# Optimization experiments

Hardware: AMD Instinct MI355X
Metric: run time of the kernel (lower is better)

Reference implementation:

```python
import jax, jax.numpy as jnp
import numpy as np

WS = 7          # window size
NH = 12         # num heads
DIM = 384       # embed dim
HD = DIM // NH  # head dim
BW = 2048       # B_ = batch * num_windows
N = WS * WS     # tokens per window


def _relative_position_index(ws):
    coords = np.stack(np.meshgrid(np.arange(ws), np.arange(ws), indexing='ij'))  # [2,ws,ws]
    cf = coords.reshape(2, -1)                      # [2, ws*ws]
    rel = cf[:, :, None] - cf[:, None, :]           # [2, N, N]
    rel = rel.transpose(1, 2, 0).copy()             # [N, N, 2]
    rel[:, :, 0] += ws - 1
    rel[:, :, 1] += ws - 1
    rel[:, :, 0] *= 2 * ws - 1
    return jnp.asarray(rel.sum(-1))                 # [N, N] int


REL_IDX = _relative_position_index(WS)


def setup_inputs() -> dict:
    key = jax.random.key(0)
    ks = jax.random.split(key, 6)
    return {
        'x': jax.random.normal(ks[0], (BW, N, DIM), dtype=jnp.float32),
        'qkv_w': jax.random.normal(ks[1], (3 * DIM, DIM), dtype=jnp.float32) * 0.02,
        'qkv_b': jax.random.normal(ks[2], (3 * DIM,), dtype=jnp.float32) * 0.02,
        'proj_w': jax.random.normal(ks[3], (DIM, DIM), dtype=jnp.float32) * 0.02,
        'proj_b': jax.random.normal(ks[4], (DIM,), dtype=jnp.float32) * 0.02,
        'rel_bias_table': jax.random.normal(ks[5], ((2 * WS - 1) ** 2, NH), dtype=jnp.float32) * 0.02,
    }


def reference(x, qkv_w, qkv_b, proj_w, proj_b, rel_bias_table):
    B_, n, c = x.shape
    scale = HD ** -0.5
    qkv = x @ qkv_w.T + qkv_b                                   # [B_, N, 3*DIM]
    qkv = qkv.reshape(B_, n, 3, NH, HD).transpose(2, 0, 3, 1, 4)  # [3, B_, H, N, HD]
    q, k, v = qkv[0], qkv[1], qkv[2]
    attn = jnp.einsum('bhnd,bhmd->bhnm', q * scale, k)           # [B_, H, N, N]
    bias = rel_bias_table[REL_IDX.reshape(-1)].reshape(n, n, NH)  # gather -> [N, N, H]
    attn = attn + bias.transpose(2, 0, 1)[None]                   # add [1, H, N, N]
    attn = jax.nn.softmax(attn, axis=-1)
    out = jnp.einsum('bhnm,bhmd->bhnd', attn, v)                 # [B_, H, N, HD]
    out = out.transpose(0, 2, 1, 3).reshape(B_, n, c)            # [B_, N, C]
    return out @ proj_w.T + proj_b
```

## Files before the change

kernel.cpp:

```cpp
#include <hip/hip_runtime.h>
#include <hip/hip_bf16.h>

#define NH 12
constexpr float SCALE = 0.17677669529663687f;
constexpr int TOKENS = 100352;

using f32x4  = __attribute__((ext_vector_type(4))) float;
using bf16x8 = __attribute__((ext_vector_type(8))) __bf16;

__device__ inline void gload_lds16(const void* g, void* l) {
  __builtin_amdgcn_global_load_lds(
      (const __attribute__((address_space(1))) void*)g,
      (__attribute__((address_space(3))) void*)l, 16, 0, 0);
}

__device__ inline bf16x8 cvt8(float4 a, float4 b) {
  bf16x8 o;
  o[0] = (__bf16)a.x; o[1] = (__bf16)a.y; o[2] = (__bf16)a.z; o[3] = (__bf16)a.w;
  o[4] = (__bf16)b.x; o[5] = (__bf16)b.y; o[6] = (__bf16)b.z; o[7] = (__bf16)b.w;
  return o;
}

#define MFMA(a, b, c) __builtin_amdgcn_mfma_f32_16x16x32_bf16(a, b, c, 0, 0, 0)

__global__ __launch_bounds__(256) void wa_prep(
    const float* __restrict__ qkv_w, const float* __restrict__ proj_w,
    const float* __restrict__ tbl,
    __bf16* __restrict__ qkv_w_bf, __bf16* __restrict__ proj_w_bf,
    float* __restrict__ biasTt) {
  int p = blockIdx.x * 256 + threadIdx.x;
  if (p < 442368) { qkv_w_bf[p] = (__bf16)qkv_w[p]; return; }
  p -= 442368;
  if (p < 147456) { proj_w_bf[p] = (__bf16)proj_w[p]; return; }
  p -= 147456;
  if (p >= 49152) return;
  int h = p >> 12, rem = p & 4095, j = rem >> 6, i = rem & 63;
  float v;
  if (j >= 49) v = -1e30f;
  else if (i >= 49) v = 0.0f;
  else {
    int py = i / 7, px = i % 7, qy = j / 7, qx = j % 7;
    v = tbl[((py - qy + 6) * 13 + (px - qx + 6)) * NH + h];
  }
  biasTt[p] = v;
}

__global__ __launch_bounds__(256, 4) void wa_qkv(
    const float* __restrict__ x, const __bf16* __restrict__ wq,
    const float* __restrict__ qkv_b, __bf16* __restrict__ qkv) {
  __shared__ __bf16 As[64 * 64];
  __shared__ __bf16 Bs[128 * 64];
  __shared__ __bf16 Cs[64 * 128];
  const int t = threadIdx.x, lane = t & 63, wv = t >> 6;
  const int lr = lane & 15, ls = lane >> 4;
  const int bid = blockIdx.x;
  const int q = bid / 72, rem = bid - q * 72;
  const int nb = rem >> 3, mb = q * 8 + (rem & 7);
  const int wr = wv >> 1, wc = wv & 1;
  f32x4 acc[2][4] = {};
  for (int kk = 0; kk < 6; ++kk) {
    if (kk) __syncthreads();
    float4 a0[2], a1[2];
    int rowA[2], cA[2];
    #pragma unroll
    for (int j = 0; j < 2; ++j) {
      int p = j * 256 + t;
      rowA[j] = p >> 3; cA[j] = p & 7;
      const float* src = x + (size_t)(mb * 64 + rowA[j]) * 384 + kk * 64 + cA[j] * 8;
      a0[j] = *(const float4*)src;
      a1[j] = *(const float4*)(src + 4);
    }
    #pragma unroll
    for (int j = 0; j < 4; ++j) {
      int p = j * 256 + t;
      int c = p >> 3, sl = p & 7;
      gload_lds16(wq + (size_t)(nb * 128 + c) * 384 + kk * 64 + (sl ^ (c & 7)) * 8,
                  Bs + p * 8);
    }
    #pragma unroll
    for (int j = 0; j < 2; ++j) {
      int cw = cA[j] ^ (rowA[j] & 7);
      *(bf16x8*)(As + rowA[j] * 64 + cw * 8) = cvt8(a0[j], a1[j]);
    }
    __syncthreads();
    #pragma unroll
    for (int ks = 0; ks < 2; ++ks) {
      bf16x8 af[2], bfr[4];
      #pragma unroll
      for (int rt = 0; rt < 2; ++rt) {
        int row = wr * 32 + rt * 16 + lr;
        af[rt] = *(const bf16x8*)(As + row * 64 + (((ks * 4 + ls) ^ (row & 7)) * 8));
      }
      #pragma unroll
      for (int ct = 0; ct < 4; ++ct) {
        int c = wc * 64 + ct * 16 + lr;
        bfr[ct] = *(const bf16x8*)(Bs + c * 64 + (((ks * 4 + ls) ^ (c & 7)) * 8));
      }
      #pragma unroll
      for (int rt = 0; rt < 2; ++rt)
        #pragma unroll
        for (int ct = 0; ct < 4; ++ct)
          acc[rt][ct] = MFMA(af[rt], bfr[ct], acc[rt][ct]);
    }
  }
  #pragma unroll
  for (int ct = 0; ct < 4; ++ct) {
    float b = qkv_b[nb * 128 + wc * 64 + ct * 16 + lr];
    #pragma unroll
    for (int rt = 0; rt < 2; ++rt)
      #pragma unroll
      for (int r = 0; r < 4; ++r) {
        int row = wr * 32 + rt * 16 + ls * 4 + r;
        Cs[row * 128 + wc * 64 + ct * 16 + lr] = (__bf16)(acc[rt][ct][r] + b);
      }
  }
  __syncthreads();
  #pragma unroll
  for (int j = 0; j < 4; ++j) {
    int p = j * 256 + t;
    int row = p >> 4, sub = p & 15;
    *(bf16x8*)(qkv + (size_t)(mb * 64 + row) * 1152 + nb * 128 + sub * 8) =
        *(const bf16x8*)(Cs + p * 8);
  }
}

__global__ __launch_bounds__(256, 3) void wa_attn(
    const float* __restrict__ biasTt, __bf16* __restrict__ qkv) {
  __shared__ __bf16 Pbuf[4][4096];
  __shared__ __bf16 Vbuf[4][2048];
  const int t = threadIdx.x, lane = t & 63, wv = t >> 6;
  const int lr = lane & 15, ls = lane >> 4;
  const int pair = blockIdx.x * 4 + wv;
  const int w = pair / NH, h = pair - w * NH;
  const int w49 = w * 49;
  __bf16* Pw = Pbuf[wv];
  __bf16* Vw = Vbuf[wv];
  f32x4 zero = {0.f, 0.f, 0.f, 0.f};
  bf16x8 ones;
  #pragma unroll
  for (int e = 0; e < 8; ++e) ones[e] = (__bf16)1.0f;

  {
    int row = lane;
    int tok = w49 + (row < 49 ? row : 48);
    const bf16x8* vsrc = (const bf16x8*)(qkv + (size_t)tok * 1152 + 768 + h * 32);
    int f = (row & 3) ^ ((row >> 3) & 3);
    #pragma unroll
    for (int c = 0; c < 4; ++c)
      *(bf16x8*)(Vw + row * 32 + ((c ^ f) * 8)) = vsrc[c];
  }
  bf16x8 qa[4], kb[4];
  #pragma unroll
  for (int rt = 0; rt < 4; ++rt) {
    int tok = min(w49 + rt * 16 + lr, TOKENS - 1);
    qa[rt] = *(const bf16x8*)(qkv + (size_t)tok * 1152 + h * 32 + ls * 8);
  }
  #pragma unroll
  for (int ct = 0; ct < 4; ++ct) {
    int tok = min(w49 + ct * 16 + lr, TOKENS - 1);
    kb[ct] = *(const bf16x8*)(qkv + (size_t)tok * 1152 + 384 + h * 32 + ls * 8);
  }
  f32x4 sacc[4][4];
  #pragma unroll
  for (int rt = 0; rt < 4; ++rt)
    #pragma unroll
    for (int ct = 0; ct < 4; ++ct)
      sacc[rt][ct] = MFMA(qa[rt], kb[ct], zero);
  #pragma unroll
  for (int rt = 0; rt < 4; ++rt) {
    int row0 = rt * 16 + ls * 4;
    #pragma unroll
    for (int ct = 0; ct < 4; ++ct) {
      int col = ct * 16 + lr;
      float4 bias = *(const float4*)(biasTt + (size_t)(h * 64 + col) * 64 + row0);
      #pragma unroll
      for (int r = 0; r < 4; ++r) {
        int row = row0 + r;
        float pr = __expf(fmaf(sacc[rt][ct][r], SCALE, ((const float*)&bias)[r]));
        Pw[row * 64 + (((col >> 3) ^ (row & 7)) * 8) + (col & 7)] = (__bf16)pr;
      }
    }
  }
  f32x4 oacc[4][2] = {};
  f32x4 osum[4] = {zero, zero, zero, zero};
  #pragma unroll
  for (int ks = 0; ks < 2; ++ks) {
    bf16x8 vb0, vb1;
    #pragma unroll
    for (int e = 0; e < 8; ++e) {
      int j = ks * 32 + ls * 8 + e;
      int a = j * 32 + (((lr >> 3) ^ (e & 3) ^ ls) * 8) + (lr & 7);
      vb0[e] = Vw[a];
      vb1[e] = Vw[a ^ 16];
    }
    #pragma unroll
    for (int rt = 0; rt < 4; ++rt) {
      int row = rt * 16 + lr;
      bf16x8 pa = *(const bf16x8*)(Pw + row * 64 + (((ks * 4 + ls) ^ (row & 7)) * 8));
      oacc[rt][0] = MFMA(pa, vb0, oacc[rt][0]);
      oacc[rt][1] = MFMA(pa, vb1, oacc[rt][1]);
      osum[rt]    = MFMA(pa, ones, osum[rt]);
    }
  }
  #pragma unroll
  for (int rt = 0; rt < 4; ++rt)
    #pragma unroll
    for (int r = 0; r < 4; ++r) {
      int row = rt * 16 + ls * 4 + r;
      if (row < 49) {
        float inv = 1.0f / osum[rt][r];
        __bf16* o = qkv + (size_t)(w49 + row) * 1152 + h * 32;
        o[lr]      = (__bf16)(oacc[rt][0][r] * inv);
        o[16 + lr] = (__bf16)(oacc[rt][1][r] * inv);
      }
    }
}

__global__ __launch_bounds__(256, 4) void wa_proj(
    const __bf16* __restrict__ qkv, const __bf16* __restrict__ pw,
    const float* __restrict__ proj_b, float* __restrict__ out) {
  __shared__ __bf16 As[64 * 64];
  __shared__ __bf16 Bs[128 * 64];
  const int t = threadIdx.x, lane = t & 63, wv = t >> 6;
  const int lr = lane & 15, ls = lane >> 4;
  const int bid = blockIdx.x;
  const int q = bid / 24, rem = bid - q * 24;
  const int nb = rem >> 3, mb = q * 8 + (rem & 7);
  const int wr = wv >> 1, wc = wv & 1;
  f32x4 acc[2][4] = {};
  for (int kk = 0; kk < 6; ++kk) {
    if (kk) __syncthreads();
    #pragma unroll
    for (int j = 0; j < 2; ++j) {
      int p = j * 256 + t;
      int row = p >> 3, sl = p & 7;
      gload_lds16(qkv + (size_t)(mb * 64 + row) * 1152 + kk * 64 + (sl ^ (row & 7)) * 8,
                  As + p * 8);
    }
    #pragma unroll
    for (int j = 0; j < 4; ++j) {
      int p = j * 256 + t;
      int c = p >> 3, sl = p & 7;
      gload_lds16(pw + (size_t)(nb * 128 + c) * 384 + kk * 64 + (sl ^ (c & 7)) * 8,
                  Bs + p * 8);
    }
    __syncthreads();
    #pragma unroll
    for (int ks = 0; ks < 2; ++ks) {
      bf16x8 af[2], bfr[4];
      #pragma unroll
      for (int rt = 0; rt < 2; ++rt) {
        int row = wr * 32 + rt * 16 + lr;
        af[rt] = *(const bf16x8*)(As + row * 64 + (((ks * 4 + ls) ^ (row & 7)) * 8));
      }
      #pragma unroll
      for (int ct = 0; ct < 4; ++ct) {
        int c = wc * 64 + ct * 16 + lr;
        bfr[ct] = *(const bf16x8*)(Bs + c * 64 + (((ks * 4 + ls) ^ (c & 7)) * 8));
      }
      #pragma unroll
      for (int rt = 0; rt < 2; ++rt)
        #pragma unroll
        for (int ct = 0; ct < 4; ++ct)
          acc[rt][ct] = MFMA(af[rt], bfr[ct], acc[rt][ct]);
    }
  }
  #pragma unroll
  for (int ct = 0; ct < 4; ++ct) {
    int col = nb * 128 + wc * 64 + ct * 16 + lr;
    float b = proj_b[col];
    #pragma unroll
    for (int rt = 0; rt < 2; ++rt)
      #pragma unroll
      for (int r = 0; r < 4; ++r) {
        int row = wr * 32 + rt * 16 + ls * 4 + r;
        out[(size_t)(mb * 64 + row) * 384 + col] = acc[rt][ct][r] + b;
      }
  }
}

extern "C" void kernel_launch(void* const* d_in, const int* in_sizes, int n_in,
                              void* d_out, int out_size, void* d_ws, size_t ws_size,
                              hipStream_t stream) {
  const float* x      = (const float*)d_in[0];
  const float* qkv_w  = (const float*)d_in[1];
  const float* qkv_b  = (const float*)d_in[2];
  const float* proj_w = (const float*)d_in[3];
  const float* proj_b = (const float*)d_in[4];
  const float* tbl    = (const float*)d_in[5];
  float* out = (float*)d_out;

  char* ws = (char*)d_ws;
  __bf16* qkv_w_bf  = (__bf16*)ws;
  __bf16* proj_w_bf = (__bf16*)(ws + 884736);
  float*  biasTt    = (float*)(ws + 1179648);
  __bf16* qkv_buf   = (__bf16*)(ws + 1376256);

  wa_prep<<<2496, 256, 0, stream>>>(qkv_w, proj_w, tbl, qkv_w_bf, proj_w_bf, biasTt);
  wa_qkv<<<14112, 256, 0, stream>>>(x, qkv_w_bf, qkv_b, qkv_buf);
  wa_attn<<<6144, 256, 0, stream>>>(biasTt, qkv_buf);
  wa_proj<<<4704, 256, 0, stream>>>(qkv_buf, proj_w_bf, proj_b, out);
}
```

Measured before the change: 336.5 us.

## Drop LDS staging in QKV and proj GEMMs, load MFMA fragments directly from global

Both projection GEMMs stop staging A and B tiles through shared memory with block-wide barriers. Each wave now loads its MFMA operand fragments straight from global memory (L2/L1) and keeps only a small per-wave LDS buffer for the coalesced output write in the QKV kernel. This removes the __syncthreads and LDS traffic per k-step, but each wave now fetches operand data that other waves in the block also fetch, and the loads are strided 16-byte per-lane rather than coalesced tiles.

```diff
diff --git a/kernel.cpp b/kernel.cpp
--- a/kernel.cpp
+++ b/kernel.cpp
@@ -7,12 +7,6 @@
 
 using f32x4  = __attribute__((ext_vector_type(4))) float;
 using bf16x8 = __attribute__((ext_vector_type(8))) __bf16;
-
-__device__ inline void gload_lds16(const void* g, void* l) {
-  __builtin_amdgcn_global_load_lds(
-      (const __attribute__((address_space(1))) void*)g,
-      (__attribute__((address_space(3))) void*)l, 16, 0, 0);
-}
 
 __device__ inline bf16x8 cvt8(float4 a, float4 b) {
   bf16x8 o;
@@ -48,79 +42,50 @@
 __global__ __launch_bounds__(256, 4) void wa_qkv(
     const float* __restrict__ x, const __bf16* __restrict__ wq,
     const float* __restrict__ qkv_b, __bf16* __restrict__ qkv) {
-  __shared__ __bf16 As[64 * 64];
-  __shared__ __bf16 Bs[128 * 64];
-  __shared__ __bf16 Cs[64 * 128];
+  __shared__ alignas(16) __bf16 Cs[4][2048];
   const int t = threadIdx.x, lane = t & 63, wv = t >> 6;
   const int lr = lane & 15, ls = lane >> 4;
   const int bid = blockIdx.x;
   const int q = bid / 72, rem = bid - q * 72;
   const int nb = rem >> 3, mb = q * 8 + (rem & 7);
   const int wr = wv >> 1, wc = wv & 1;
+  const float*  xb = x  + (size_t)(mb * 64 + wr * 32) * 384;
+  const __bf16* wb = wq + (size_t)(nb * 128 + wc * 64) * 384;
+
   f32x4 acc[2][4] = {};
-  for (int kk = 0; kk < 6; ++kk) {
-    if (kk) __syncthreads();
-    float4 a0[2], a1[2];
-    int rowA[2], cA[2];
-    #pragma unroll
-    for (int j = 0; j < 2; ++j) {
-      int p = j * 256 + t;
-      rowA[j] = p >> 3; cA[j] = p & 7;
-      const float* src = x + (size_t)(mb * 64 + rowA[j]) * 384 + kk * 64 + cA[j] * 8;
-      a0[j] = *(const float4*)src;
-      a1[j] = *(const float4*)(src + 4);
-    }
-    #pragma unroll
-    for (int j = 0; j < 4; ++j) {
-      int p = j * 256 + t;
-      int c = p >> 3, sl = p & 7;
-      gload_lds16(wq + (size_t)(nb * 128 + c) * 384 + kk * 64 + (sl ^ (c & 7)) * 8,
-                  Bs + p * 8);
-    }
-    #pragma unroll
-    for (int j = 0; j < 2; ++j) {
-      int cw = cA[j] ^ (rowA[j] & 7);
-      *(bf16x8*)(As + rowA[j] * 64 + cw * 8) = cvt8(a0[j], a1[j]);
-    }
-    __syncthreads();
-    #pragma unroll
-    for (int ks = 0; ks < 2; ++ks) {
-      bf16x8 af[2], bfr[4];
-      #pragma unroll
-      for (int rt = 0; rt < 2; ++rt) {
-        int row = wr * 32 + rt * 16 + lr;
-        af[rt] = *(const bf16x8*)(As + row * 64 + (((ks * 4 + ls) ^ (row & 7)) * 8));
-      }
-      #pragma unroll
-      for (int ct = 0; ct < 4; ++ct) {
-        int c = wc * 64 + ct * 16 + lr;
-        bfr[ct] = *(const bf16x8*)(Bs + c * 64 + (((ks * 4 + ls) ^ (c & 7)) * 8));
-      }
-      #pragma unroll
-      for (int rt = 0; rt < 2; ++rt)
-        #pragma unroll
-        for (int ct = 0; ct < 4; ++ct)
-          acc[rt][ct] = MFMA(af[rt], bfr[ct], acc[rt][ct]);
-    }
-  }
+  #pragma unroll 3
+  for (int kc = 0; kc < 12; ++kc) {
+    bf16x8 af[2], bfr[4];
+    #pragma unroll
+    for (int rt = 0; rt < 2; ++rt) {
+      const float* p = xb + (size_t)(rt * 16 + lr) * 384 + kc * 32 + ls * 8;
+      af[rt] = cvt8(*(const float4*)p, *(const float4*)(p + 4));
+    }
+    #pragma unroll
+    for (int ct = 0; ct < 4; ++ct)
+      bfr[ct] = *(const bf16x8*)(wb + (size_t)(ct * 16 + lr) * 384 + kc * 32 + ls * 8);
+    #pragma unroll
+    for (int rt = 0; rt < 2; ++rt)
+      #pragma unroll
+      for (int ct = 0; ct < 4; ++ct)
+        acc[rt][ct] = MFMA(af[rt], bfr[ct], acc[rt][ct]);
+  }
+  __bf16* C = Cs[wv];
   #pragma unroll
   for (int ct = 0; ct < 4; ++ct) {
     float b = qkv_b[nb * 128 + wc * 64 + ct * 16 + lr];
     #pragma unroll
     for (int rt = 0; rt < 2; ++rt)
       #pragma unroll
-      for (int r = 0; r < 4; ++r) {
-        int row = wr * 32 + rt * 16 + ls * 4 + r;
-        Cs[row * 128 + wc * 64 + ct * 16 + lr] = (__bf16)(acc[rt][ct][r] + b);
-      }
-  }
-  __syncthreads();
-  #pragma unroll
-  for (int j = 0; j < 4; ++j) {
-    int p = j * 256 + t;
-    int row = p >> 4, sub = p & 15;
-    *(bf16x8*)(qkv + (size_t)(mb * 64 + row) * 1152 + nb * 128 + sub * 8) =
-        *(const bf16x8*)(Cs + p * 8);
+      for (int r = 0; r < 4; ++r)
+        C[(rt * 16 + ls * 4 + r) * 64 + ct * 16 + lr] = (__bf16)(acc[rt][ct][r] + b);
+  }
+  #pragma unroll
+  for (int i = 0; i < 4; ++i) {
+    int p = i * 64 + lane;
+    int row = p >> 3, sub = p & 7;
+    *(bf16x8*)(qkv + (size_t)(mb * 64 + wr * 32 + row) * 1152 + nb * 128 + wc * 64 + sub * 8) =
+        *(const bf16x8*)(C + row * 64 + sub * 8);
   }
 }
 
@@ -219,51 +184,30 @@
 __global__ __launch_bounds__(256, 4) void wa_proj(
     const __bf16* __restrict__ qkv, const __bf16* __restrict__ pw,
     const float* __restrict__ proj_b, float* __restrict__ out) {
-  __shared__ __bf16 As[64 * 64];
-  __shared__ __bf16 Bs[128 * 64];
   const int t = threadIdx.x, lane = t & 63, wv = t >> 6;
   const int lr = lane & 15, ls = lane >> 4;
   const int bid = blockIdx.x;
   const int q = bid / 24, rem = bid - q * 24;
   const int nb = rem >> 3, mb = q * 8 + (rem & 7);
   const int wr = wv >> 1, wc = wv & 1;
+  const __bf16* ab = qkv + (size_t)(mb * 64 + wr * 32) * 1152;
+  const __bf16* wb = pw  + (size_t)(nb * 128 + wc * 64) * 384;
+
   f32x4 acc[2][4] = {};
-  for (int kk = 0; kk < 6; ++kk) {
-    if (kk) __syncthreads();
-    #pragma unroll
-    for (int j = 0; j < 2; ++j) {
-      int p = j * 256 + t;
-      int row = p >> 3, sl = p & 7;
-      gload_lds16(qkv + (size_t)(mb * 64 + row) * 1152 + kk * 64 + (sl ^ (row & 7)) * 8,
-                  As + p * 8);
-    }
-    #pragma unroll
-    for (int j = 0; j < 4; ++j) {
-      int p = j * 256 + t;
-      int c = p >> 3, sl = p & 7;
-      gload_lds16(pw + (size_t)(nb * 128 + c) * 384 + kk * 64 + (sl ^ (c & 7)) * 8,
-                  Bs + p * 8);
-    }
-    __syncthreads();
-    #pragma unroll
-    for (int ks = 0; ks < 2; ++ks) {
-      bf16x8 af[2], bfr[4];
-      #pragma unroll
-      for (int rt = 0; rt < 2; ++rt) {
-        int row = wr * 32 + rt * 16 + lr;
-        af[rt] = *(const bf16x8*)(As + row * 64 + (((ks * 4 + ls) ^ (row & 7)) * 8));
-      }
-      #pragma unroll
-      for (int ct = 0; ct < 4; ++ct) {
-        int c = wc * 64 + ct * 16 + lr;
-        bfr[ct] = *(const bf16x8*)(Bs + c * 64 + (((ks * 4 + ls) ^ (c & 7)) * 8));
-      }
-      #pragma unroll
-      for (int rt = 0; rt < 2; ++rt)
-        #pragma unroll
-        for (int ct = 0; ct < 4; ++ct)
-          acc[rt][ct] = MFMA(af[rt], bfr[ct], acc[rt][ct]);
-    }
+  #pragma unroll 3
+  for (int kc = 0; kc < 12; ++kc) {
+    bf16x8 af[2], bfr[4];
+    #pragma unroll
+    for (int rt = 0; rt < 2; ++rt)
+      af[rt] = *(const bf16x8*)(ab + (size_t)(rt * 16 + lr) * 1152 + kc * 32 + ls * 8);
+    #pragma unroll
+    for (int ct = 0; ct < 4; ++ct)
+      bfr[ct] = *(const bf16x8*)(wb + (size_t)(ct * 16 + lr) * 384 + kc * 32 + ls * 8);
+    #pragma unroll
+    for (int rt = 0; rt < 2; ++rt)
+      #pragma unroll
+      for (int ct = 0; ct < 4; ++ct)
+        acc[rt][ct] = MFMA(af[rt], bfr[ct], acc[rt][ct]);
   }
   #pragma unroll
   for (int ct = 0; ct < 4; ++ct) {
```

Measured after the change: 868.9 us. +158.2%, slower.
